# Optimization experiments

Measured on AMD Instinct MI355X. Metric: run time of the kernel, lower is better.

Reference implementation:

```python
import jax, jax.numpy as jnp
import numpy as np

TOP_K = 128
HID = 256


def _mlp2(h, w1, b1, w2, b2):
    return jax.nn.relu(h @ w1 + b1) @ w2 + b2


def setup_inputs() -> dict:
    key = jax.random.key(0)
    ks = jax.random.split(key, 20)
    B, L, D = 512, 256, 64
    s = 0.05
    inp = {
        "x": jax.random.normal(ks[0], (B, L, D), dtype=jnp.float32),
        "Wq": jax.random.normal(ks[1], (D, HID)) * s, "bq": jnp.zeros((HID,)),
        "Wk": jax.random.normal(ks[2], (D, HID)) * s, "bk": jnp.zeros((HID,)),
        "phi_w1": jax.random.normal(ks[3], (D, HID)) * s, "phi_b1": jnp.zeros((HID,)),
        "phi_w2": jax.random.normal(ks[4], (HID, HID)) * s, "phi_b2": jnp.zeros((HID,)),
        "xi_w1": jax.random.normal(ks[5], (2 * D, HID)) * s, "xi_b1": jnp.zeros((HID,)),
        "xi_w2": jax.random.normal(ks[6], (HID, HID)) * s, "xi_b2": jnp.zeros((HID,)),
        "rho_w1": jax.random.normal(ks[7], (HID, HID)) * s, "rho_b1": jnp.zeros((HID,)),
        "rho_w2": jax.random.normal(ks[8], (HID, 128)) * s, "rho_b2": jnp.zeros((128,)),
    }
    return inp


def reference(x, Wq, bq, Wk, bk, phi_w1, phi_b1, phi_w2, phi_b2,
              xi_w1, xi_b1, xi_w2, xi_b2, rho_w1, rho_b1, rho_w2, rho_b2):
    B, L, D = x.shape
    scale = HID ** (-0.5)
    # padding mask (all True for randn input; trim is identity with static shapes)
    pad = jnp.sum(jnp.abs(x), axis=-1) != 0  # [B, L]
    Q = x @ Wq + bq  # [B, L, H]
    K = x @ Wk + bk
    scores = jnp.einsum("blh,bmh->blm", Q, K) * scale  # [B, L, L]
    mask2d = pad[:, :, None] & pad[:, None, :]
    scores = jnp.where(mask2d, scores, -jnp.inf)
    flat = scores.reshape(B, L * L)
    k = min(TOP_K, L * L)
    topk_vals, topk_idx = jax.lax.top_k(flat, k)  # [B, k]
    topk_w = jax.nn.softmax(topk_vals, axis=-1)
    row = topk_idx // L
    col = topk_idx % L
    x_i = jnp.take_along_axis(x, row[:, :, None], axis=1)  # [B, k, D]
    x_j = jnp.take_along_axis(x, col[:, :, None], axis=1)
    feat_self = _mlp2(x_i, phi_w1, phi_b1, phi_w2, phi_b2)  # [B, k, H]
    feat_pair = _mlp2(jnp.concatenate([x_i, x_j], axis=-1), xi_w1, xi_b1, xi_w2, xi_b2)
    self_mask = (row == col)[:, :, None]
    interaction = jnp.where(self_mask, feat_self, feat_pair)
    pooled = jnp.sum(interaction * topk_w[:, :, None], axis=1)  # [B, H]
    return _mlp2(pooled, rho_w1, rho_b1, rho_w2, rho_b2)  # [B, 128]
```

## Files before the change

### kernel.cpp

```cpp
#include <hip/hip_runtime.h>

typedef unsigned short u16;
typedef unsigned int   u32;
typedef unsigned char  u8;
typedef unsigned long long u64;

#define B_TOT 512
#define L_SEQ 256
#define D_IN  64
#define HIDN  256
#define TOPK  128
#define CAP   160
#define NWT   32
#define FLDS  76304

typedef float  f32x4  __attribute__((ext_vector_type(4)));
typedef __bf16 bf16x8 __attribute__((ext_vector_type(8)));

__device__ __forceinline__ u16 f2bf(float f){
  u32 u = __float_as_uint(f);
  u32 r = u + 0x7fffu + ((u>>16)&1u);
  return (u16)(r>>16);
}
__device__ __forceinline__ u32 sortKey(float f){
  u32 b = __float_as_uint(f);
  return (b & 0x80000000u) ? ~b : (b | 0x80000000u);
}
__device__ __forceinline__ float unKey(u32 u){
  u32 b = (u & 0x80000000u) ? (u & 0x7fffffffu) : ~u;
  return __uint_as_float(b);
}
__device__ __forceinline__ void cvt8(const float* v, u32* hp, u32* lp){
  #pragma unroll
  for (int i=0;i<4;++i){
    float v0 = v[2*i], v1 = v[2*i+1];
    u16 h0 = f2bf(v0); float h0f = __uint_as_float(((u32)h0)<<16); u16 l0 = f2bf(v0 - h0f);
    u16 h1 = f2bf(v1); float h1f = __uint_as_float(((u32)h1)<<16); u16 l1 = f2bf(v1 - h1f);
    hp[i] = (u32)h0 | ((u32)h1<<16);
    lp[i] = (u32)l0 | ((u32)l1<<16);
  }
}

__global__ __launch_bounds__(256) void k_wprep(
    const float* __restrict__ Wq, const float* __restrict__ bq,
    const float* __restrict__ Wk, const float* __restrict__ bk,
    const float* __restrict__ xi_w1, const float* __restrict__ phi_w1,
    u16* __restrict__ MtH, u16* __restrict__ MtL, float* __restrict__ uvc,
    u16* __restrict__ xiH, u16* __restrict__ xiL,
    u16* __restrict__ phiH, u16* __restrict__ phiL)
{
  int bid = blockIdx.x, tid = threadIdx.x;
  if (bid < 64){
    __shared__ float wq[HIDN];
    __shared__ float part[256];
    int a = bid;
    wq[tid] = Wq[a*HIDN + tid];
    __syncthreads();
    int bcol = tid & 63, q = tid >> 6;
    float s = 0.f;
    for (int h = q*64; h < q*64 + 64; ++h)
      s = fmaf(wq[h], Wk[bcol*HIDN + h], s);
    part[tid] = s;
    __syncthreads();
    if (tid < 64){
      float mv = part[tid] + part[64+tid] + part[128+tid] + part[192+tid];
      u16 hh = f2bf(mv); float hf = __uint_as_float(((u32)hh)<<16);
      u16 ll = f2bf(mv - hf);
      MtH[tid*64 + a] = hh;
      MtL[tid*64 + a] = ll;
    }
    int wv = tid >> 6, ln = tid & 63;
    if (wv == 0){
      float s2 = 0.f;
      #pragma unroll
      for (int i=0;i<4;++i){ int h = ln*4+i; s2 = fmaf(wq[h], bk[h], s2); }
      #pragma unroll
      for (int off=1; off<64; off<<=1) s2 += __shfl_xor(s2, off);
      if (ln == 0) uvc[a] = s2;
    } else if (wv == 1){
      float s2 = 0.f;
      #pragma unroll
      for (int i=0;i<4;++i){ int h = ln*4+i; s2 = fmaf(Wk[a*HIDN + h], bq[h], s2); }
      #pragma unroll
      for (int off=1; off<64; off<<=1) s2 += __shfl_xor(s2, off);
      if (ln == 0) uvc[64 + a] = s2;
    } else if (wv == 2 && a == 0){
      float s2 = 0.f;
      #pragma unroll
      for (int i=0;i<4;++i){ int h = ln*4+i; s2 = fmaf(bq[h], bk[h], s2); }
      #pragma unroll
      for (int off=1; off<64; off<<=1) s2 += __shfl_xor(s2, off);
      if (ln == 0) uvc[128] = s2;
    }
  } else {
    int t = (bid-64)*256 + tid;
    if (t < 256*128){
      int h = t >> 7, d = t & 127;
      float v = xi_w1[d*HIDN + h];
      u16 hh = f2bf(v); float hf = __uint_as_float(((u32)hh)<<16);
      u16 ll = f2bf(v - hf);
      xiH[h*128 + d] = hh; xiL[h*128 + d] = ll;
    } else {
      int t2 = t - 256*128;
      int h = t2 >> 6, d = t2 & 63;
      float v = phi_w1[d*HIDN + h];
      u16 hh = f2bf(v); float hf = __uint_as_float(((u32)hh)<<16);
      u16 ll = f2bf(v - hf);
      phiH[h*64 + d] = hh; phiL[h*64 + d] = ll;
    }
  }
}

__global__ void __launch_bounds__(1024) __attribute__((amdgpu_waves_per_eu(4))) k_fused(
    const float* __restrict__ x, const u16* __restrict__ MtH, const u16* __restrict__ MtL,
    const float* __restrict__ uvc,
    u64* __restrict__ cand, int* __restrict__ cand_n, u32* __restrict__ uthr)
{
  extern __shared__ __align__(16) u16 smem[];
  u16* XH = smem;
  u16* XL = XH + 256*72;
  float* STS = (float*)(XL + 256*72);
  float* STT = STS + 256;
  float* SUV = STT + 256;

  int tid = threadIdx.x;
  int b = blockIdx.x;
  const float* xb = x + (size_t)b*(L_SEQ*D_IN);

  if (tid < 129) SUV[tid] = uvc[tid];

  int ar = tid >> 2, aq = tid & 3;
  float v[16];
  {
    const float* src = xb + (size_t)ar*D_IN + aq*16;
    #pragma unroll
    for (int i=0;i<4;++i) *(float4*)&v[i*4] = *(const float4*)(src + i*4);
    u32 hpA[4],lpA[4],hpB[4],lpB[4];
    cvt8(&v[0], hpA, lpA); cvt8(&v[8], hpB, lpB);
    u16* dh = XH + ar*72 + aq*16;
    u16* dl = XL + ar*72 + aq*16;
    *(uint4*)(dh)     = make_uint4(hpA[0],hpA[1],hpA[2],hpA[3]);
    *(uint4*)(dh + 8) = make_uint4(hpB[0],hpB[1],hpB[2],hpB[3]);
    *(uint4*)(dl)     = make_uint4(lpA[0],lpA[1],lpA[2],lpA[3]);
    *(uint4*)(dl + 8) = make_uint4(lpB[0],lpB[1],lpB[2],lpB[3]);
  }
  __syncthreads();

  {
    float su=0.f, tv=0.f, pa=0.f;
    #pragma unroll
    for (int d=0; d<16; ++d){
      float xa = v[d];
      su = fmaf(xa, SUV[aq*16+d], su);
      tv = fmaf(xa, SUV[64+aq*16+d], tv);
      pa += fabsf(xa);
    }
    su += __shfl_xor(su,1); su += __shfl_xor(su,2);
    tv += __shfl_xor(tv,1); tv += __shfl_xor(tv,2);
    pa += __shfl_xor(pa,1); pa += __shfl_xor(pa,2);
    if (aq == 0){
      bool pad = (pa != 0.f);
      STS[ar] = pad ? (su + SUV[128]) : -1e38f;
      STT[ar] = pad ? tv : -1e38f;
    }
  }
  __syncthreads();

  int w = tid >> 6, lane = tid & 63, lm = lane & 15, quad = lane >> 4;
  int u  = w;
  int r0 = u*16;

  bf16x8 Yh0, Yh1, Yl0, Yl1;
  {
    const u16* xh_ = XH + (r0+lm)*72;
    const u16* xl_ = XL + (r0+lm)*72;
    bf16x8 Xh0 = *(const bf16x8*)(xh_ + quad*8);
    bf16x8 Xh1 = *(const bf16x8*)(xh_ + 32 + quad*8);
    bf16x8 Xl0 = *(const bf16x8*)(xl_ + quad*8);
    bf16x8 Xl1 = *(const bf16x8*)(xl_ + 32 + quad*8);
    u32 yh[8], yl[8];
    #pragma unroll
    for (int ct=0; ct<4; ++ct){
      int srow = 8*(lm>>2) + 4*(ct&1) + (lm&3) + 32*(ct>>1);
      const u16* mth = MtH + srow*64 + quad*8;
      const u16* mtl = MtL + srow*64 + quad*8;
      bf16x8 Mh0 = *(const bf16x8*)(mth);
      bf16x8 Mh1 = *(const bf16x8*)(mth + 32);
      bf16x8 Ml0 = *(const bf16x8*)(mtl);
      bf16x8 Ml1 = *(const bf16x8*)(mtl + 32);
      f32x4 a1 = {0.f,0.f,0.f,0.f}, a2 = {0.f,0.f,0.f,0.f};
      a1 = __builtin_amdgcn_mfma_f32_16x16x32_bf16(Mh0, Xh0, a1, 0,0,0);
      a2 = __builtin_amdgcn_mfma_f32_16x16x32_bf16(Mh1, Xh1, a2, 0,0,0);
      a1 = __builtin_amdgcn_mfma_f32_16x16x32_bf16(Ml0, Xh0, a1, 0,0,0);
      a2 = __builtin_amdgcn_mfma_f32_16x16x32_bf16(Ml1, Xh1, a2, 0,0,0);
      a1 = __builtin_amdgcn_mfma_f32_16x16x32_bf16(Mh0, Xl0, a1, 0,0,0);
      a2 = __builtin_amdgcn_mfma_f32_16x16x32_bf16(Mh1, Xl1, a2, 0,0,0);
      #pragma unroll
      for (int pr=0; pr<2; ++pr){
        float v0 = a1[2*pr]   + a2[2*pr];
        float v1 = a1[2*pr+1] + a2[2*pr+1];
        u16 h0 = f2bf(v0); u16 h1 = f2bf(v1);
        u16 l0 = f2bf(v0 - __uint_as_float(((u32)h0)<<16));
        u16 l1 = f2bf(v1 - __uint_as_float(((u32)h1)<<16));
        int slot = (ct>>1)*4 + (ct&1)*2 + pr;
        yh[slot] = (u32)h0 | ((u32)h1<<16);
        yl[slot] = (u32)l0 | ((u32)l1<<16);
      }
    }
    uint4 t0 = make_uint4(yh[0],yh[1],yh[2],yh[3]);
    uint4 t1 = make_uint4(yh[4],yh[5],yh[6],yh[7]);
    uint4 t2 = make_uint4(yl[0],yl[1],yl[2],yl[3]);
    uint4 t3 = make_uint4(yl[4],yl[5],yl[6],yl[7]);
    Yh0 = *(const bf16x8*)&t0;
    Yh1 = *(const bf16x8*)&t1;
    Yl0 = *(const bf16x8*)&t2;
    Yl1 = *(const bf16x8*)&t3;
  }

  float sr[4];
  #pragma unroll
  for (int r=0;r<4;++r) sr[r] = STS[r0 + quad*4 + r];

  for (int ch=0; ch<2; ++ch){
    int j0 = ch*128;
    u32 kv[32];
    #pragma unroll
    for (int ct=0; ct<8; ++ct){
      const u16* bh = XH + (j0 + ct*16+lm)*72;
      const u16* bl = XL + (j0 + ct*16+lm)*72;
      bf16x8 Bh0 = *(const bf16x8*)(bh + quad*8);
      bf16x8 Bh1 = *(const bf16x8*)(bh + 32 + quad*8);
      bf16x8 Bl0 = *(const bf16x8*)(bl + quad*8);
      bf16x8 Bl1 = *(const bf16x8*)(bl + 32 + quad*8);
      f32x4 a1 = {0.f,0.f,0.f,0.f}, a2 = {0.f,0.f,0.f,0.f};
      a1 = __builtin_amdgcn_mfma_f32_16x16x32_bf16(Yh0, Bh0, a1, 0,0,0);
      a2 = __builtin_amdgcn_mfma_f32_16x16x32_bf16(Yh1, Bh1, a2, 0,0,0);
      a1 = __builtin_amdgcn_mfma_f32_16x16x32_bf16(Yl0, Bh0, a1, 0,0,0);
      a2 = __builtin_amdgcn_mfma_f32_16x16x32_bf16(Yl1, Bh1, a2, 0,0,0);
      a1 = __builtin_amdgcn_mfma_f32_16x16x32_bf16(Yh0, Bl0, a1, 0,0,0);
      a2 = __builtin_amdgcn_mfma_f32_16x16x32_bf16(Yh1, Bl1, a2, 0,0,0);
      float tc = STT[j0 + ct*16 + lm];
      #pragma unroll
      for (int r=0;r<4;++r)
        kv[ct*4 + r] = sortKey(a1[r] + a2[r] + sr[r] + tc);
    }

    u32 T = 0;
    for (int bit=15; bit>=0; --bit){
      u32 th2 = (T | (1u<<bit)) << 16;
      int c0 = 0, c1 = 0;
      #pragma unroll
      for (int i=0;i<32;i+=2){
        c0 += (int)__popcll(__ballot(kv[i]   >= th2));
        c1 += (int)__popcll(__ballot(kv[i+1] >= th2));
      }
      int c = c0 + c1;
      if (c >= TOPK){
        T |= (1u<<bit);
        if (c <= CAP) break;
      }
    }
    u32 thr = T << 16;
    u32 up  = (T < 0xffffu) ? ((T+1u) << 16) : 0xffffffffu;

    u32 m1 = 0, m2 = 0;
    #pragma unroll
    for (int i=0;i<32;++i){
      bool ge = kv[i] >= thr;
      bool c1 = ge && (kv[i] >= up);
      m1 |= (c1 ? 1u : 0u) << i;
      m2 |= ((ge && !c1) ? 1u : 0u) << i;
    }
    int n1 = __popc(m1), n2 = __popc(m2);
    int p1 = n1, p2 = n2;
    #pragma unroll
    for (int off=1; off<64; off<<=1){
      int a = __shfl_up(p1, off); if (lane >= off) p1 += a;
      int c = __shfl_up(p2, off); if (lane >= off) p2 += c;
    }
    int tot1 = __shfl(p1, 63), tot2 = __shfl(p2, 63);
    int pos1 = p1 - n1;
    int pos2 = tot1 + (p2 - n2);
    int total = tot1 + tot2;
    int wt = u*2 + ch;
    size_t base = ((size_t)b*NWT + wt)*CAP;
    if (lane == 0){
      cand_n[b*NWT + wt] = (total < CAP) ? total : CAP;
      uthr[b*NWT + wt] = thr;
    }
    {
      int o1=0, o2=0;
      #pragma unroll
      for (int i=0;i<32;++i){
        bool c1 = (m1 >> i) & 1u, c2v = (m2 >> i) & 1u;
        if (c1 | c2v){
          int p = c1 ? (pos1 + o1) : (pos2 + o2);
          int flat = (r0 + quad*4 + (i&3))*L_SEQ + (j0 + (i>>2)*16 + lm);
          if (p < CAP) cand[base + p] = ((u64)kv[i] << 32) | (u32)flat;
        }
        o1 += c1; o2 += c2v;
      }
    }
  }
}

__global__ __launch_bounds__(256) void k_pre(
    const float* __restrict__ x, const u16* __restrict__ MtH, const u16* __restrict__ MtL,
    const float* __restrict__ uvc,
    u16* __restrict__ xh, u16* __restrict__ xl,
    u16* __restrict__ yh, u16* __restrict__ yl,
    float* __restrict__ st)
{
  __shared__ __align__(16) u16 sh[64][72];
  __shared__ __align__(16) u16 sl[64][72];
  __shared__ float sUV[132];
  int tid = threadIdx.x;
  int g0 = blockIdx.x * 64;
  int b  = g0 >> 8, l0 = g0 & 255;
  int r = tid >> 2, q = tid & 3;

  if (tid < 129) sUV[tid] = uvc[tid];

  float v[16];
  {
    const float* xr = x + (size_t)(g0 + r)*D_IN + q*16;
    #pragma unroll
    for (int i=0;i<4;++i) *(float4*)&v[i*4] = *(const float4*)(xr + i*4);
  }
  {
    u32 hpA[4],lpA[4],hpB[4],lpB[4];
    cvt8(&v[0], hpA, lpA); cvt8(&v[8], hpB, lpB);
    size_t xo = (size_t)(g0 + r)*D_IN + q*16;
    *(uint4*)(xh + xo)     = make_uint4(hpA[0],hpA[1],hpA[2],hpA[3]);
    *(uint4*)(xh + xo + 8) = make_uint4(hpB[0],hpB[1],hpB[2],hpB[3]);
    *(uint4*)(xl + xo)     = make_uint4(lpA[0],lpA[1],lpA[2],lpA[3]);
    *(uint4*)(xl + xo + 8) = make_uint4(lpB[0],lpB[1],lpB[2],lpB[3]);
    *(uint4*)&sh[r][q*16]   = make_uint4(hpA[0],hpA[1],hpA[2],hpA[3]);
    *(uint4*)&sh[r][q*16+8] = make_uint4(hpB[0],hpB[1],hpB[2],hpB[3]);
    *(uint4*)&sl[r][q*16]   = make_uint4(lpA[0],lpA[1],lpA[2],lpA[3]);
    *(uint4*)&sl[r][q*16+8] = make_uint4(lpB[0],lpB[1],lpB[2],lpB[3]);
  }
  __syncthreads();

  {
    float su=0.f, tv=0.f, pa=0.f;
    #pragma unroll
    for (int d=0; d<16; ++d){
      float xa = v[d];
      su = fmaf(xa, sUV[q*16+d], su);
      tv = fmaf(xa, sUV[64+q*16+d], tv);
      pa += fabsf(xa);
    }
    su += __shfl_xor(su,1); su += __shfl_xor(su,2);
    tv += __shfl_xor(tv,1); tv += __shfl_xor(tv,2);
    pa += __shfl_xor(pa,1); pa += __shfl_xor(pa,2);
    if (q == 0){
      bool pad = (pa != 0.f);
      st[(size_t)b*L_SEQ + l0 + r]          = pad ? (su + sUV[128]) : -1e38f;
      st[(size_t)(B_TOT+b)*L_SEQ + l0 + r]  = pad ? tv : -1e38f;
    }
  }

  int w = tid >> 6, lane = tid & 63, lm = lane & 15, quad = lane >> 4;
  bf16x8 Ah0 = *(const bf16x8*)&sh[w*16+lm][quad*8];
  bf16x8 Ah1 = *(const bf16x8*)&sh[w*16+lm][32 + quad*8];
  bf16x8 Al0 = *(const bf16x8*)&sl[w*16+lm][quad*8];
  bf16x8 Al1 = *(const bf16x8*)&sl[w*16+lm][32 + quad*8];
  #pragma unroll
  for (int ct=0; ct<4; ++ct){
    const u16* mth = MtH + (ct*16+lm)*64 + quad*8;
    const u16* mtl = MtL + (ct*16+lm)*64 + quad*8;
    bf16x8 Bh0 = *(const bf16x8*)(mth);
    bf16x8 Bh1 = *(const bf16x8*)(mth + 32);
    bf16x8 Bl0 = *(const bf16x8*)(mtl);
    bf16x8 Bl1 = *(const bf16x8*)(mtl + 32);
    f32x4 a1 = {0.f,0.f,0.f,0.f}, a2 = {0.f,0.f,0.f,0.f};
    a1 = __builtin_amdgcn_mfma_f32_16x16x32_bf16(Ah0, Bh0, a1, 0,0,0);
    a2 = __builtin_amdgcn_mfma_f32_16x16x32_bf16(Ah1, Bh1, a2, 0,0,0);
    a1 = __builtin_amdgcn_mfma_f32_16x16x32_bf16(Al0, Bh0, a1, 0,0,0);
    a2 = __builtin_amdgcn_mfma_f32_16x16x32_bf16(Al1, Bh1, a2, 0,0,0);
    a1 = __builtin_amdgcn_mfma_f32_16x16x32_bf16(Ah0, Bl0, a1, 0,0,0);
    a2 = __builtin_amdgcn_mfma_f32_16x16x32_bf16(Ah1, Bl1, a2, 0,0,0);
    #pragma unroll
    for (int rg=0; rg<4; ++rg){
      float vy = a1[rg] + a2[rg];
      u16 hh = f2bf(vy); float hf = __uint_as_float(((u32)hh)<<16);
      u16 ll = f2bf(vy - hf);
      sh[w*16 + quad*4 + rg][ct*16 + lm] = hh;
      sl[w*16 + quad*4 + rg][ct*16 + lm] = ll;
    }
  }
  {
    size_t yo = (size_t)(g0 + r)*D_IN + q*16;
    *(uint4*)(yh + yo)     = *(uint4*)&sh[r][q*16];
    *(uint4*)(yh + yo + 8) = *(uint4*)&sh[r][q*16+8];
    *(uint4*)(yl + yo)     = *(uint4*)&sl[r][q*16];
    *(uint4*)(yl + yo + 8) = *(uint4*)&sl[r][q*16+8];
  }
}

__global__ __launch_bounds__(256) void k_score(
    const u16* __restrict__ xh, const u16* __restrict__ xl,
    const u16* __restrict__ yh, const u16* __restrict__ yl,
    const float* __restrict__ st,
    u64* __restrict__ cand, int* __restrict__ cand_n, u32* __restrict__ uthr)
{
  int tid = threadIdx.x;
  int lin = blockIdx.x;
  int b    = ((lin >> 6) << 3) | (lin & 7);
  int tile = (lin >> 3) & 7;
  int cb = tile & 1, rb = tile >> 1;
  int r0 = rb*64, j0 = cb*128;
  int w = tid >> 6, lane = tid & 63, lm = lane & 15, quad = lane >> 4;

  size_t rowA = ((size_t)b*L_SEQ + r0 + w*16 + lm)*D_IN;
  bf16x8 A_h0 = *(const bf16x8*)(yh + rowA + quad*8);
  bf16x8 A_h1 = *(const bf16x8*)(yh + rowA + 32 + quad*8);
  bf16x8 A_l0 = *(const bf16x8*)(yl + rowA + quad*8);
  bf16x8 A_l1 = *(const bf16x8*)(yl + rowA + 32 + quad*8);

  float4 s4 = *(const float4*)(st + (size_t)b*L_SEQ + r0 + w*16 + quad*4);
  float sr[4] = {s4.x, s4.y, s4.z, s4.w};
  float tc[8];
  #pragma unroll
  for (int ct=0;ct<8;++ct)
    tc[ct] = st[(size_t)(B_TOT + b)*L_SEQ + j0 + ct*16 + lm];

  u32 kv[32];
  #pragma unroll
  for (int ct=0; ct<8; ++ct){
    size_t rowB = ((size_t)b*L_SEQ + j0 + ct*16 + lm)*D_IN;
    bf16x8 B_h0 = *(const bf16x8*)(xh + rowB + quad*8);
    bf16x8 B_h1 = *(const bf16x8*)(xh + rowB + 32 + quad*8);
    bf16x8 B_l0 = *(const bf16x8*)(xl + rowB + quad*8);
    bf16x8 B_l1 = *(const bf16x8*)(xl + rowB + 32 + quad*8);
    f32x4 a1 = {0.f,0.f,0.f,0.f}, a2 = {0.f,0.f,0.f,0.f};
    a1 = __builtin_amdgcn_mfma_f32_16x16x32_bf16(A_h0, B_h0, a1, 0,0,0);
    a2 = __builtin_amdgcn_mfma_f32_16x16x32_bf16(A_h1, B_h1, a2, 0,0,0);
    a1 = __builtin_amdgcn_mfma_f32_16x16x32_bf16(A_l0, B_h0, a1, 0,0,0);
    a2 = __builtin_amdgcn_mfma_f32_16x16x32_bf16(A_l1, B_h1, a2, 0,0,0);
    a1 = __builtin_amdgcn_mfma_f32_16x16x32_bf16(A_h0, B_l0, a1, 0,0,0);
    a2 = __builtin_amdgcn_mfma_f32_16x16x32_bf16(A_h1, B_l1, a2, 0,0,0);
    #pragma unroll
    for (int r=0;r<4;++r)
      kv[ct*4 + r] = sortKey(a1[r] + a2[r] + sr[r] + tc[ct]);
  }

  u32 T = 0;
  for (int bit=15; bit>=0; --bit){
    u32 th2 = (T | (1u<<bit)) << 16;
    int c = 0;
    #pragma unroll
    for (int i=0;i<32;++i)
      c += (int)__popcll(__ballot(kv[i] >= th2));
    if (c >= TOPK){
      T |= (1u<<bit);
      if (c <= CAP) break;
    }
  }
  u32 thr = T << 16;

  u32 hm = 0;
  #pragma unroll
  for (int i=0;i<32;++i) hm |= (kv[i] >= thr ? 1u : 0u) << i;
  int myc = __popc(hm);
  int pre = myc;
  #pragma unroll
  for (int off=1; off<64; off<<=1){
    int n = __shfl_up(pre, off);
    if (lane >= off) pre += n;
  }
  int total = __shfl(pre, 63);
  int pos = pre - myc;
  int wt = tile*4 + w;
  size_t base = ((size_t)b*NWT + wt)*CAP;
  if (lane == 0){
    cand_n[b*NWT + wt] = (total < CAP) ? total : CAP;
    uthr[b*NWT + wt] = thr;
  }
  while (hm){
    int i = __ffs(hm) - 1; hm &= hm - 1;
    if (pos < CAP){
      int r = i & 3, ct = i >> 2;
      int flat = (r0 + w*16 + quad*4 + r)*L_SEQ + (j0 + ct*16 + lm);
      cand[base + pos] = ((u64)kv[i] << 32) | (u32)flat;
    }
    ++pos;
  }
}

__global__ __launch_bounds__(256) void k_merge(
    const u64* __restrict__ cand, const int* __restrict__ cand_n, const u32* __restrict__ uthr,
    int* __restrict__ selidx, float* __restrict__ selw)
{
  const int SL   = NWT/4;
  const int NSW  = SL*CAP/64;
  const int WCAP = 192;
  __shared__ u64 wbuf[4][WCAP];
  __shared__ int wcnt[4];
  __shared__ int scnt[NWT];
  __shared__ u32 wT[4];
  __shared__ int cm, eqc;
  __shared__ int eqi[256];
  __shared__ float sv[TOPK]; __shared__ int si[TOPK];
  __shared__ float fred[8];
  int b = blockIdx.x, tid = threadIdx.x;
  int w = tid >> 6, lane = tid & 63;
  if (tid < NWT) scnt[tid] = cand_n[b*NWT + tid];
  if (tid == 0){ cm = 0; eqc = 0; }
  __syncthreads();

  u32 key[NSW]; int idx[NSW];
  size_t bb = (size_t)b*NWT*CAP + (size_t)(w*SL)*CAP;
  #pragma unroll
  for (int s=0;s<NSW;++s){
    int e = lane + 64*s;
    int slot = e / CAP, p = e - slot*CAP;
    bool ok = p < scnt[w*SL + slot];
    u64 v = ok ? cand[bb + e] : 0ull;
    key[s] = (u32)(v >> 32);
    idx[s] = ok ? (int)(u32)v : 0x7fffffff;
  }

  u32 lb = uthr[b*NWT + w*SL + (lane & 7)];
  #pragma unroll
  for (int off=1; off<8; off<<=1){
    u32 o = (u32)__shfl_xor((int)lb, off);
    lb = lb > o ? lb : o;
  }

  u32 T = 0;
  for (int bit=31; bit>=0; --bit){
    u32 c2 = T | (1u<<bit);
    if (c2 <= lb){ T = c2; continue; }
    int c = 0;
    #pragma unroll
    for (int s=0;s<NSW;++s) c += (int)__popcll(__ballot(key[s] >= c2));
    if (c >= TOPK){
      T = c2;
      if (c <= WCAP) break;
    }
  }
  if (lane == 0) wT[w] = T;
  {
    int myc = 0;
    #pragma unroll
    for (int s=0;s<NSW;++s) myc += (key[s] >= T) ? 1 : 0;
    int pre = myc;
    #pragma unroll
    for (int off=1; off<64; off<<=1){
      int n = __shfl_up(pre, off);
      if (lane >= off) pre += n;
    }
    int total = __shfl(pre, 63);
    int pos = pre - myc;
    if (lane == 0) wcnt[w] = (total < WCAP) ? total : WCAP;
    #pragma unroll
    for (int s=0;s<NSW;++s){
      if (key[s] >= T){
        if (pos < WCAP) wbuf[w][pos] = ((u64)key[s] << 32) | (u32)idx[s];
        ++pos;
      }
    }
  }
  __syncthreads();

  if (w == 0){
    const int NS2 = 4*WCAP/64;
    u32 k2[NS2]; int i2[NS2];
    #pragma unroll
    for (int s=0;s<NS2;++s){
      int e = lane + 64*s;
      int slot = e / WCAP, p = e - slot*WCAP;
      bool ok = p < wcnt[slot];
      u64 v = ok ? wbuf[slot][p] : 0ull;
      k2[s] = (u32)(v >> 32);
      i2[s] = ok ? (int)(u32)v : 0x7fffffff;
    }
    u32 lb2 = wT[0];
    lb2 = lb2 > wT[1] ? lb2 : wT[1];
    lb2 = lb2 > wT[2] ? lb2 : wT[2];
    lb2 = lb2 > wT[3] ? lb2 : wT[3];
    u32 T2 = 0;
    for (int bit=31; bit>=0; --bit){
      u32 c2 = T2 | (1u<<bit);
      if (c2 <= lb2){ T2 = c2; continue; }
      int c = 0;
      #pragma unroll
      for (int s=0;s<NS2;++s) c += (int)__popcll(__ballot(k2[s] >= c2));
      if (c >= TOPK) T2 = c2;
    }
    int m = 0;
    #pragma unroll
    for (int s=0;s<NS2;++s) m += (int)__popcll(__ballot(k2[s] > T2));
    #pragma unroll
    for (int s=0;s<NS2;++s){
      if (k2[s] > T2){
        int p = atomicAdd(&cm, 1);
        sv[p] = unKey(k2[s]) * 0.0625f; si[p] = i2[s];
      } else if (k2[s] == T2 && i2[s] != 0x7fffffff){
        int q = atomicAdd(&eqc, 1);
        if (q < 256) eqi[q] = i2[s];
      }
    }
    if (lane == 0){
      int need = TOPK - m;
      int n = eqc < 256 ? eqc : 256;
      float tv = unKey(T2) * 0.0625f;
      for (int s2=0; s2<need; ++s2){
        int bi = s2;
        for (int j=s2+1;j<n;++j) if (eqi[j] < eqi[bi]) bi = j;
        int t2 = eqi[s2]; eqi[s2] = eqi[bi]; eqi[bi] = t2;
        sv[m+s2] = tv; si[m+s2] = eqi[s2];
      }
    }
  }
  __syncthreads();

  float v = (tid < TOPK) ? sv[tid] : -3.4e38f;
  float mx = v;
  #pragma unroll
  for (int off=1; off<64; off<<=1) mx = fmaxf(mx, __shfl_xor(mx, off));
  if ((tid&63)==0) fred[tid>>6] = mx;
  __syncthreads();
  mx = fmaxf(fred[0], fred[1]);
  float e = (tid < TOPK) ? expf(v - mx) : 0.f;
  float s = e;
  #pragma unroll
  for (int off=1; off<64; off<<=1) s += __shfl_xor(s, off);
  if ((tid&63)==0) fred[4 + (tid>>6)] = s;
  __syncthreads();
  s = fred[4] + fred[5];
  if (tid < TOPK){
    selw[(size_t)b*TOPK + tid]   = e / s;
    selidx[(size_t)b*TOPK + tid] = si[tid];
  }
}

__global__ __launch_bounds__(512) void k_mlp(
    const float* __restrict__ x, const int* __restrict__ selidx, const float* __restrict__ selw,
    const u16* __restrict__ xiH, const u16* __restrict__ xiL,
    const u16* __restrict__ phiH, const u16* __restrict__ phiL,
    const float* __restrict__ phi_b1, const float* __restrict__ phi_w2, const float* __restrict__ phi_b2,
    const float* __restrict__ xi_b1,  const float* __restrict__ xi_w2,  const float* __restrict__ xi_b2,
    const float* __restrict__ rho_w1, const float* __restrict__ rho_b1,
    const float* __restrict__ rho_w2, const float* __restrict__ rho_b2,
    float* __restrict__ out)
{
  __shared__ __align__(16) u16 AFh[8][4][64][8];
  __shared__ __align__(16) u16 AFl[8][4][64][8];
  __shared__ int   sidx[TOPK];
  __shared__ float swp[TOPK], swd[TOPK];
  __shared__ float gpL[256], gsL[256];
  __shared__ float pooled[256], t1[256];
  __shared__ float pp[512];
  __shared__ float wsums[2];
  int b = blockIdx.x, tid = threadIdx.x;
  int w = tid >> 6, lane = tid & 63;

  if (tid < TOPK){
    int fl = selidx[(size_t)b*TOPK + tid];
    sidx[tid] = fl;
    float wv = selw[(size_t)b*TOPK + tid];
    bool dg = ((fl>>8) == (fl&255));
    swp[tid] = dg ? 0.f : wv;
    swd[tid] = dg ? wv  : 0.f;
  }
  __syncthreads();

  if (w == 0){
    float a = swp[lane] + swp[64 + lane];
    #pragma unroll
    for (int off=1; off<64; off<<=1) a += __shfl_xor(a, off);
    if (lane == 0) wsums[0] = a;
  } else if (w == 1){
    float a = swd[lane] + swd[64 + lane];
    #pragma unroll
    for (int off=1; off<64; off<<=1) a += __shfl_xor(a, off);
    if (lane == 0) wsums[1] = a;
  }

  {
    int m = tid >> 2, qq = tid & 3;
    int fl = sidx[m];
    int rc = (qq < 2) ? (fl >> 8) : (fl & 255);
    const float* src = x + ((size_t)b*L_SEQ + rc)*D_IN + (qq & 1)*32;
    int kt = m >> 4, l16 = m & 15;
    #pragma unroll
    for (int g=0; g<4; ++g){
      float v[8];
      *(float4*)&v[0] = *(const float4*)(src + g*8);
      *(float4*)&v[4] = *(const float4*)(src + g*8 + 4);
      u32 hp[4], lp[4];
      cvt8(v, hp, lp);
      *(uint4*)&AFh[kt][qq][l16 + 16*g][0] = make_uint4(hp[0],hp[1],hp[2],hp[3]);
      *(uint4*)&AFl[kt][qq][l16 + 16*g][0] = make_uint4(lp[0],lp[1],lp[2],lp[3]);
    }
  }
  __syncthreads();

  int lm = lane & 15, quad = lane >> 4;

  #pragma unroll
  for (int hi2=0; hi2<2; ++hi2){
    int ht = w + 8*hi2;
    int h  = ht*16 + lm;
    bf16x8 BXh[4], BXl[4], BPh[2], BPl[2];
    #pragma unroll
    for (int c=0;c<4;++c){
      BXh[c] = *(const bf16x8*)(xiH + h*128 + c*32 + quad*8);
      BXl[c] = *(const bf16x8*)(xiL + h*128 + c*32 + quad*8);
    }
    #pragma unroll
    for (int c=0;c<2;++c){
      BPh[c] = *(const bf16x8*)(phiH + h*64 + c*32 + quad*8);
      BPl[c] = *(const bf16x8*)(phiL + h*64 + c*32 + quad*8);
    }
    float bxi = xi_b1[h], bph = phi_b1[h];
    float gp = 0.f, gs = 0.f;
    for (int kt=0; kt<8; ++kt){
      bf16x8 Ah_[4], Al_[4];
      #pragma unroll
      for (int c=0;c<4;++c){
        Ah_[c] = *(const bf16x8*)&AFh[kt][c][lane][0];
        Al_[c] = *(const bf16x8*)&AFl[kt][c][lane][0];
      }
      f32x4 cx = {0.f,0.f,0.f,0.f}, cp = {0.f,0.f,0.f,0.f};
      #pragma unroll
      for (int c=0;c<4;++c){
        cx = __builtin_amdgcn_mfma_f32_16x16x32_bf16(Ah_[c], BXh[c], cx, 0,0,0);
        cx = __builtin_amdgcn_mfma_f32_16x16x32_bf16(Al_[c], BXh[c], cx, 0,0,0);
        cx = __builtin_amdgcn_mfma_f32_16x16x32_bf16(Ah_[c], BXl[c], cx, 0,0,0);
      }
      #pragma unroll
      for (int c=0;c<2;++c){
        cp = __builtin_amdgcn_mfma_f32_16x16x32_bf16(Ah_[c], BPh[c], cp, 0,0,0);
        cp = __builtin_amdgcn_mfma_f32_16x16x32_bf16(Al_[c], BPh[c], cp, 0,0,0);
        cp = __builtin_amdgcn_mfma_f32_16x16x32_bf16(Ah_[c], BPl[c], cp, 0,0,0);
      }
      #pragma unroll
      for (int r=0;r<4;++r){
        int kk = kt*16 + quad*4 + r;
        gp = fmaf(swp[kk], fmaxf(cx[r] + bxi, 0.f), gp);
        gs = fmaf(swd[kk], fmaxf(cp[r] + bph, 0.f), gs);
      }
    }
    gp += __shfl_xor(gp, 16); gp += __shfl_xor(gp, 32);
    gs += __shfl_xor(gs, 16); gs += __shfl_xor(gs, 32);
    if (quad == 0){ gpL[h] = gp; gsL[h] = gs; }
  }
  __syncthreads();

  {
    int h = tid & 255, half = tid >> 8;
    float wsp = wsums[0], wss = wsums[1];
    float po = (half == 0) ? (wsp*xi_b2[h] + wss*phi_b2[h]) : 0.f;
    int dd0 = half*128;
    for (int d=dd0; d<dd0+128; ++d){
      po = fmaf(gpL[d], xi_w2[d*HIDN + h], po);
      po = fmaf(gsL[d], phi_w2[d*HIDN + h], po);
    }
    pp[half*256 + h] = po;
  }
  __syncthreads();
  if (tid < 256) pooled[tid] = pp[tid] + pp[256 + tid];
  __syncthreads();
  {
    int h = tid & 255, half = tid >> 8;
    float a = (half == 0) ? rho_b1[h] : 0.f;
    int dd0 = half*128;
    for (int d=dd0; d<dd0+128; ++d) a = fmaf(pooled[d], rho_w1[d*HIDN + h], a);
    pp[half*256 + h] = a;
  }
  __syncthreads();
  if (tid < 256) t1[tid] = fmaxf(pp[tid] + pp[256 + tid], 0.f);
  __syncthreads();
  {
    int h = tid & 127, part = tid >> 7;
    float o = (part == 0) ? rho_b2[h] : 0.f;
    int dd0 = part*64;
    for (int d=dd0; d<dd0+64; ++d) o = fmaf(t1[d], rho_w2[d*128 + h], o);
    pp[part*128 + h] = o;
  }
  __syncthreads();
  if (tid < 128)
    out[(size_t)b*128 + tid] = pp[tid] + pp[128+tid] + pp[256+tid] + pp[384+tid];
}

extern "C" void kernel_launch(void* const* d_in, const int* in_sizes, int n_in,
                              void* d_out, int out_size, void* d_ws, size_t ws_size,
                              hipStream_t stream)
{
  (void)in_sizes; (void)n_in; (void)out_size; (void)ws_size;
  const float* x      = (const float*)d_in[0];
  const float* Wq     = (const float*)d_in[1];
  const float* bq     = (const float*)d_in[2];
  const float* Wk     = (const float*)d_in[3];
  const float* bk     = (const float*)d_in[4];
  const float* phi_w1 = (const float*)d_in[5];
  const float* phi_b1 = (const float*)d_in[6];
  const float* phi_w2 = (const float*)d_in[7];
  const float* phi_b2 = (const float*)d_in[8];
  const float* xi_w1  = (const float*)d_in[9];
  const float* xi_b1  = (const float*)d_in[10];
  const float* xi_w2  = (const float*)d_in[11];
  const float* xi_b2  = (const float*)d_in[12];
  const float* rho_w1 = (const float*)d_in[13];
  const float* rho_b1 = (const float*)d_in[14];
  const float* rho_w2 = (const float*)d_in[15];
  const float* rho_b2 = (const float*)d_in[16];
  float* out = (float*)d_out;

  const size_t NX = (size_t)B_TOT*L_SEQ*D_IN;
  float* uvc    = (float*)d_ws;
  float* st     = uvc + 256;
  float* selw   = st + (size_t)2*B_TOT*L_SEQ;
  int*   selidx = (int*)(selw + (size_t)B_TOT*TOPK);
  int*   cand_n = selidx + (size_t)B_TOT*TOPK;
  u32*   uthr   = (u32*)(cand_n + (size_t)B_TOT*NWT);
  u64*   cand   = (u64*)(uthr + (size_t)B_TOT*NWT);
  u16*   MtH    = (u16*)(cand + (size_t)B_TOT*NWT*CAP);
  u16*   MtL    = MtH + 64*64;
  u16*   xiH    = MtL + 64*64;
  u16*   xiL    = xiH + 256*128;
  u16*   phiH   = xiL + 256*128;
  u16*   phiL   = phiH + 256*64;
  u16*   xh     = phiL + 256*64;
  u16*   xl     = xh + NX;
  u16*   yh     = xl + NX;
  u16*   yl     = yh + NX;

  hipError_t aerr = hipFuncSetAttribute((const void*)k_fused,
                      hipFuncAttributeMaxDynamicSharedMemorySize, FLDS);

  k_wprep<<<dim3(256),  dim3(256), 0, stream>>>(Wq, bq, Wk, bk, xi_w1, phi_w1,
                                                MtH, MtL, uvc, xiH, xiL, phiH, phiL);
  if (aerr == hipSuccess){
    k_fused<<<dim3(B_TOT), dim3(1024), FLDS, stream>>>(x, MtH, MtL, uvc, cand, cand_n, uthr);
  } else {
    k_pre  <<<dim3(2048), dim3(256), 0, stream>>>(x, MtH, MtL, uvc, xh, xl, yh, yl, st);
    k_score<<<dim3(4096), dim3(256), 0, stream>>>(xh, xl, yh, yl, st, cand, cand_n, uthr);
  }
  k_merge<<<dim3(B_TOT), dim3(256), 0, stream>>>(cand, cand_n, uthr, selidx, selw);
  k_mlp  <<<dim3(B_TOT), dim3(512), 0, stream>>>(x, selidx, selw,
            xiH, xiL, phiH, phiL,
            phi_b1, phi_w2, phi_b2,
            xi_b1, xi_w2, xi_b2,
            rho_w1, rho_b1, rho_w2, rho_b2, out);
}
```

Before: 250.6 us.

## Fuse top-k merge kernel into MLP kernel and pin fused waves per EU

Moves the per-batch candidate merge, threshold selection and softmax from a separate k_merge launch into the start of k_mlp, reusing the AFh shared buffer as scratch for the wave buffers and tie list. This drops one kernel launch and the global round-trip of selidx/selw. It also sets amdgpu_waves_per_eu(4,4) on k_fused to fix its occupancy target. The cost is that only 4 of k_mlp's 8 waves do the merge work, and the merge now adds its shared-memory and register needs to the MLP kernel, which may lower that kernel's occupancy.

```diff
diff --git a/kernel.cpp b/kernel.cpp
--- a/kernel.cpp
+++ b/kernel.cpp
@@ -111,7 +111,7 @@
   }
 }
 
-__global__ void __launch_bounds__(1024) __attribute__((amdgpu_waves_per_eu(4))) k_fused(
+__global__ void __launch_bounds__(1024) __attribute__((amdgpu_waves_per_eu(4,4))) k_fused(
     const float* __restrict__ x, const u16* __restrict__ MtH, const u16* __restrict__ MtL,
     const float* __restrict__ uvc,
     u64* __restrict__ cand, int* __restrict__ cand_n, u32* __restrict__ uthr)
@@ -489,156 +489,9 @@
   }
 }
 
-__global__ __launch_bounds__(256) void k_merge(
+__global__ __launch_bounds__(512) void k_mlp(
+    const float* __restrict__ x,
     const u64* __restrict__ cand, const int* __restrict__ cand_n, const u32* __restrict__ uthr,
-    int* __restrict__ selidx, float* __restrict__ selw)
-{
-  const int SL   = NWT/4;
-  const int NSW  = SL*CAP/64;
-  const int WCAP = 192;
-  __shared__ u64 wbuf[4][WCAP];
-  __shared__ int wcnt[4];
-  __shared__ int scnt[NWT];
-  __shared__ u32 wT[4];
-  __shared__ int cm, eqc;
-  __shared__ int eqi[256];
-  __shared__ float sv[TOPK]; __shared__ int si[TOPK];
-  __shared__ float fred[8];
-  int b = blockIdx.x, tid = threadIdx.x;
-  int w = tid >> 6, lane = tid & 63;
-  if (tid < NWT) scnt[tid] = cand_n[b*NWT + tid];
-  if (tid == 0){ cm = 0; eqc = 0; }
-  __syncthreads();
-
-  u32 key[NSW]; int idx[NSW];
-  size_t bb = (size_t)b*NWT*CAP + (size_t)(w*SL)*CAP;
-  #pragma unroll
-  for (int s=0;s<NSW;++s){
-    int e = lane + 64*s;
-    int slot = e / CAP, p = e - slot*CAP;
-    bool ok = p < scnt[w*SL + slot];
-    u64 v = ok ? cand[bb + e] : 0ull;
-    key[s] = (u32)(v >> 32);
-    idx[s] = ok ? (int)(u32)v : 0x7fffffff;
-  }
-
-  u32 lb = uthr[b*NWT + w*SL + (lane & 7)];
-  #pragma unroll
-  for (int off=1; off<8; off<<=1){
-    u32 o = (u32)__shfl_xor((int)lb, off);
-    lb = lb > o ? lb : o;
-  }
-
-  u32 T = 0;
-  for (int bit=31; bit>=0; --bit){
-    u32 c2 = T | (1u<<bit);
-    if (c2 <= lb){ T = c2; continue; }
-    int c = 0;
-    #pragma unroll
-    for (int s=0;s<NSW;++s) c += (int)__popcll(__ballot(key[s] >= c2));
-    if (c >= TOPK){
-      T = c2;
-      if (c <= WCAP) break;
-    }
-  }
-  if (lane == 0) wT[w] = T;
-  {
-    int myc = 0;
-    #pragma unroll
-    for (int s=0;s<NSW;++s) myc += (key[s] >= T) ? 1 : 0;
-    int pre = myc;
-    #pragma unroll
-    for (int off=1; off<64; off<<=1){
-      int n = __shfl_up(pre, off);
-      if (lane >= off) pre += n;
-    }
-    int total = __shfl(pre, 63);
-    int pos = pre - myc;
-    if (lane == 0) wcnt[w] = (total < WCAP) ? total : WCAP;
-    #pragma unroll
-    for (int s=0;s<NSW;++s){
-      if (key[s] >= T){
-        if (pos < WCAP) wbuf[w][pos] = ((u64)key[s] << 32) | (u32)idx[s];
-        ++pos;
-      }
-    }
-  }
-  __syncthreads();
-
-  if (w == 0){
-    const int NS2 = 4*WCAP/64;
-    u32 k2[NS2]; int i2[NS2];
-    #pragma unroll
-    for (int s=0;s<NS2;++s){
-      int e = lane + 64*s;
-      int slot = e / WCAP, p = e - slot*WCAP;
-      bool ok = p < wcnt[slot];
-      u64 v = ok ? wbuf[slot][p] : 0ull;
-      k2[s] = (u32)(v >> 32);
-      i2[s] = ok ? (int)(u32)v : 0x7fffffff;
-    }
-    u32 lb2 = wT[0];
-    lb2 = lb2 > wT[1] ? lb2 : wT[1];
-    lb2 = lb2 > wT[2] ? lb2 : wT[2];
-    lb2 = lb2 > wT[3] ? lb2 : wT[3];
-    u32 T2 = 0;
-    for (int bit=31; bit>=0; --bit){
-      u32 c2 = T2 | (1u<<bit);
-      if (c2 <= lb2){ T2 = c2; continue; }
-      int c = 0;
-      #pragma unroll
-      for (int s=0;s<NS2;++s) c += (int)__popcll(__ballot(k2[s] >= c2));
-      if (c >= TOPK) T2 = c2;
-    }
-    int m = 0;
-    #pragma unroll
-    for (int s=0;s<NS2;++s) m += (int)__popcll(__ballot(k2[s] > T2));
-    #pragma unroll
-    for (int s=0;s<NS2;++s){
-      if (k2[s] > T2){
-        int p = atomicAdd(&cm, 1);
-        sv[p] = unKey(k2[s]) * 0.0625f; si[p] = i2[s];
-      } else if (k2[s] == T2 && i2[s] != 0x7fffffff){
-        int q = atomicAdd(&eqc, 1);
-        if (q < 256) eqi[q] = i2[s];
-      }
-    }
-    if (lane == 0){
-      int need = TOPK - m;
-      int n = eqc < 256 ? eqc : 256;
-      float tv = unKey(T2) * 0.0625f;
-      for (int s2=0; s2<need; ++s2){
-        int bi = s2;
-        for (int j=s2+1;j<n;++j) if (eqi[j] < eqi[bi]) bi = j;
-        int t2 = eqi[s2]; eqi[s2] = eqi[bi]; eqi[bi] = t2;
-        sv[m+s2] = tv; si[m+s2] = eqi[s2];
-      }
-    }
-  }
-  __syncthreads();
-
-  float v = (tid < TOPK) ? sv[tid] : -3.4e38f;
-  float mx = v;
-  #pragma unroll
-  for (int off=1; off<64; off<<=1) mx = fmaxf(mx, __shfl_xor(mx, off));
-  if ((tid&63)==0) fred[tid>>6] = mx;
-  __syncthreads();
-  mx = fmaxf(fred[0], fred[1]);
-  float e = (tid < TOPK) ? expf(v - mx) : 0.f;
-  float s = e;
-  #pragma unroll
-  for (int off=1; off<64; off<<=1) s += __shfl_xor(s, off);
-  if ((tid&63)==0) fred[4 + (tid>>6)] = s;
-  __syncthreads();
-  s = fred[4] + fred[5];
-  if (tid < TOPK){
-    selw[(size_t)b*TOPK + tid]   = e / s;
-    selidx[(size_t)b*TOPK + tid] = si[tid];
-  }
-}
-
-__global__ __launch_bounds__(512) void k_mlp(
-    const float* __restrict__ x, const int* __restrict__ selidx, const float* __restrict__ selw,
     const u16* __restrict__ xiH, const u16* __restrict__ xiL,
     const u16* __restrict__ phiH, const u16* __restrict__ phiL,
     const float* __restrict__ phi_b1, const float* __restrict__ phi_w2, const float* __restrict__ phi_b2,
@@ -651,20 +504,165 @@
   __shared__ __align__(16) u16 AFl[8][4][64][8];
   __shared__ int   sidx[TOPK];
   __shared__ float swp[TOPK], swd[TOPK];
+  __shared__ float sv[TOPK]; __shared__ int si[TOPK];
   __shared__ float gpL[256], gsL[256];
   __shared__ float pooled[256], t1[256];
   __shared__ float pp[512];
+  __shared__ float fred[16];
   __shared__ float wsums[2];
+  __shared__ int   scnt[NWT];
+  __shared__ int   cmx[2];
+  __shared__ u32   wT[4];
+  __shared__ int   wcnt[4];
+
+  u64* wbuf = (u64*)&AFh[0][0][0][0];
+  int* eqi  = (int*)(wbuf + 4*192);
+
+  const int SL   = NWT/4;
+  const int NSW  = SL*CAP/64;
+  const int WCAP = 192;
+
   int b = blockIdx.x, tid = threadIdx.x;
   int w = tid >> 6, lane = tid & 63;
 
-  if (tid < TOPK){
-    int fl = selidx[(size_t)b*TOPK + tid];
-    sidx[tid] = fl;
-    float wv = selw[(size_t)b*TOPK + tid];
-    bool dg = ((fl>>8) == (fl&255));
-    swp[tid] = dg ? 0.f : wv;
-    swd[tid] = dg ? wv  : 0.f;
+  if (tid < NWT) scnt[tid] = cand_n[b*NWT + tid];
+  if (tid == 0){ cmx[0] = 0; cmx[1] = 0; }
+  __syncthreads();
+
+  if (w < 4){
+    u32 key[NSW]; int idx[NSW];
+    size_t bb = (size_t)b*NWT*CAP + (size_t)(w*SL)*CAP;
+    #pragma unroll
+    for (int s=0;s<NSW;++s){
+      int e = lane + 64*s;
+      int slot = e / CAP, p = e - slot*CAP;
+      bool ok = p < scnt[w*SL + slot];
+      u64 v = ok ? cand[bb + e] : 0ull;
+      key[s] = (u32)(v >> 32);
+      idx[s] = ok ? (int)(u32)v : 0x7fffffff;
+    }
+
+    u32 lb = uthr[b*NWT + w*SL + (lane & 7)];
+    #pragma unroll
+    for (int off=1; off<8; off<<=1){
+      u32 o = (u32)__shfl_xor((int)lb, off);
+      lb = lb > o ? lb : o;
+    }
+
+    u32 T = 0;
+    for (int bit=31; bit>=0; --bit){
+      u32 c2 = T | (1u<<bit);
+      if (c2 <= lb){ T = c2; continue; }
+      int c = 0;
+      #pragma unroll
+      for (int s=0;s<NSW;++s) c += (int)__popcll(__ballot(key[s] >= c2));
+      if (c >= TOPK){
+        T = c2;
+        if (c <= WCAP) break;
+      }
+    }
+    if (lane == 0) wT[w] = T;
+    int myc = 0;
+    #pragma unroll
+    for (int s=0;s<NSW;++s) myc += (key[s] >= T) ? 1 : 0;
+    int pre = myc;
+    #pragma unroll
+    for (int off=1; off<64; off<<=1){
+      int n = __shfl_up(pre, off);
+      if (lane >= off) pre += n;
+    }
+    int total = __shfl(pre, 63);
+    int pos = pre - myc;
+    if (lane == 0) wcnt[w] = (total < WCAP) ? total : WCAP;
+    #pragma unroll
+    for (int s=0;s<NSW;++s){
+      if (key[s] >= T){
+        if (pos < WCAP) wbuf[w*WCAP + pos] = ((u64)key[s] << 32) | (u32)idx[s];
+        ++pos;
+      }
+    }
+  }
+  __syncthreads();
+
+  if (w == 0){
+    const int NS2 = 4*WCAP/64;
+    u32 k2[NS2]; int i2[NS2];
+    #pragma unroll
+    for (int s=0;s<NS2;++s){
+      int e = lane + 64*s;
+      int slot = e / WCAP, p = e - slot*WCAP;
+      bool ok = p < wcnt[slot];
+      u64 v = ok ? wbuf[slot*WCAP + p] : 0ull;
+      k2[s] = (u32)(v >> 32);
+      i2[s] = ok ? (int)(u32)v : 0x7fffffff;
+    }
+    u32 lb2 = wT[0];
+    lb2 = lb2 > wT[1] ? lb2 : wT[1];
+    lb2 = lb2 > wT[2] ? lb2 : wT[2];
+    lb2 = lb2 > wT[3] ? lb2 : wT[3];
+    u32 T2 = 0;
+    for (int bit=31; bit>=0; --bit){
+      u32 c2 = T2 | (1u<<bit);
+      if (c2 <= lb2){ T2 = c2; continue; }
+      int c = 0;
+      #pragma unroll
+      for (int s=0;s<NS2;++s) c += (int)__popcll(__ballot(k2[s] >= c2));
+      if (c >= TOPK) T2 = c2;
+    }
+    int m = 0;
+    #pragma unroll
+    for (int s=0;s<NS2;++s) m += (int)__popcll(__ballot(k2[s] > T2));
+    #pragma unroll
+    for (int s=0;s<NS2;++s){
+      if (k2[s] > T2){
+        int p = atomicAdd(&cmx[0], 1);
+        sv[p] = unKey(k2[s]) * 0.0625f; si[p] = i2[s];
+      } else if (k2[s] == T2 && i2[s] != 0x7fffffff){
+        int q = atomicAdd(&cmx[1], 1);
+        if (q < 256) eqi[q] = i2[s];
+      }
+    }
+    if (lane == 0){
+      int need = TOPK - m;
+      int n = cmx[1] < 256 ? cmx[1] : 256;
+      float tv = unKey(T2) * 0.0625f;
+      for (int s2=0; s2<need; ++s2){
+        int bi = s2;
+        for (int j=s2+1;j<n;++j) if (eqi[j] < eqi[bi]) bi = j;
+        int t2 = eqi[s2]; eqi[s2] = eqi[bi]; eqi[bi] = t2;
+        sv[m+s2] = tv; si[m+s2] = eqi[s2];
+      }
+    }
+  }
+  __syncthreads();
+
+  {
+    float vv = (tid < TOPK) ? sv[tid] : -3.4e38f;
+    float mx = vv;
+    #pragma unroll
+    for (int off=1; off<64; off<<=1) mx = fmaxf(mx, __shfl_xor(mx, off));
+    if (lane == 0) fred[w] = mx;
+    __syncthreads();
+    mx = fred[0];
+    #pragma unroll
+    for (int t=1;t<8;++t) mx = fmaxf(mx, fred[t]);
+    float e = (tid < TOPK) ? expf(vv - mx) : 0.f;
+    float sum = e;
+    #pragma unroll
+    for (int off=1; off<64; off<<=1) sum += __shfl_xor(sum, off);
+    if (lane == 0) fred[8 + w] = sum;
+    __syncthreads();
+    float s = 0.f;
+    #pragma unroll
+    for (int t=0;t<8;++t) s += fred[8+t];
+    if (tid < TOPK){
+      float wv = e / s;
+      int fl = si[tid];
+      sidx[tid] = fl;
+      bool dg = ((fl>>8) == (fl&255));
+      swp[tid] = dg ? 0.f : wv;
+      swd[tid] = dg ? wv  : 0.f;
+    }
   }
   __syncthreads();
 
@@ -814,9 +812,7 @@
   const size_t NX = (size_t)B_TOT*L_SEQ*D_IN;
   float* uvc    = (float*)d_ws;
   float* st     = uvc + 256;
-  float* selw   = st + (size_t)2*B_TOT*L_SEQ;
-  int*   selidx = (int*)(selw + (size_t)B_TOT*TOPK);
-  int*   cand_n = selidx + (size_t)B_TOT*TOPK;
+  int*   cand_n = (int*)(st + (size_t)2*B_TOT*L_SEQ);
   u32*   uthr   = (u32*)(cand_n + (size_t)B_TOT*NWT);
   u64*   cand   = (u64*)(uthr + (size_t)B_TOT*NWT);
   u16*   MtH    = (u16*)(cand + (size_t)B_TOT*NWT*CAP);
@@ -841,8 +837,7 @@
     k_pre  <<<dim3(2048), dim3(256), 0, stream>>>(x, MtH, MtL, uvc, xh, xl, yh, yl, st);
     k_score<<<dim3(4096), dim3(256), 0, stream>>>(xh, xl, yh, yl, st, cand, cand_n, uthr);
   }
-  k_merge<<<dim3(B_TOT), dim3(256), 0, stream>>>(cand, cand_n, uthr, selidx, selw);
-  k_mlp  <<<dim3(B_TOT), dim3(512), 0, stream>>>(x, selidx, selw,
+  k_mlp  <<<dim3(B_TOT), dim3(512), 0, stream>>>(x, cand, cand_n, uthr,
             xiH, xiL, phiH, phiL,
             phi_b1, phi_w2, phi_b2,
             xi_b1, xi_w2, xi_b2,
```

Result: slower. 268.3 us (+7.1%).
